# Performance work log

Hardware: AMD Instinct MI355X
Metric: run time of the kernel (lower is better)

The kernel has to match this reference:

```python
import jax, jax.numpy as jnp
import numpy as np
import math

B, L, IN_K, IN_V = 4, 2048, 256, 256
HID, HEADS, OUT = 1024, 8, 256
D = HID // HEADS  # head_dim = 128


def setup_inputs() -> dict:
    key = jax.random.key(0)
    ks = jax.random.split(key, 9)
    s = 0.02
    return {
        "KEY": jax.random.normal(ks[0], (B, L, IN_K), jnp.float32),
        "VALUE": jax.random.normal(ks[1], (B, L, IN_V), jnp.float32),
        "QUERY": jax.random.normal(ks[2], (B, L, IN_K), jnp.float32),
        "W_w": jax.random.normal(ks[3], (HID, IN_K), jnp.float32) * s,
        "W_b": jax.random.normal(ks[4], (HID,), jnp.float32) * s,
        "Wv_w": jax.random.normal(ks[5], (HID, IN_V), jnp.float32) * s,
        "Wv_b": jax.random.normal(ks[6], (HID,), jnp.float32) * s,
        "Wo_w": jax.random.normal(ks[7], (OUT, HID), jnp.float32) * s,
        "Wo_b": jax.random.normal(ks[8], (OUT,), jnp.float32) * s,
    }


def _split_heads(x, b, l):
    # reshape hidden -> (head_dim, num_heads) [head LAST, as in source], then
    # permute(0,3,1,2) -> [B, heads, L, head_dim]
    return x.reshape(b, l, D, HEADS).transpose(0, 3, 1, 2)


def reference(KEY, VALUE, QUERY, W_w, W_b, Wv_w, Wv_b, Wo_w, Wo_b):
    b, lk, _ = KEY.shape
    lq = QUERY.shape[1]
    # shared projection W for KEY and QUERY
    Wk = _split_heads(KEY @ W_w.T + W_b, b, lk)      # [B,h,Lk,d]
    Wq = _split_heads(QUERY @ W_w.T + W_b, b, lq)    # [B,h,Lq,d]
    Wv = _split_heads(VALUE @ Wv_w.T + Wv_b, b, lk)  # [B,h,Lk,d]
    # score[b,h,i,k] = sum_j Wk[b,h,i,j] * Wq[b,h,k,j]
    score = jnp.einsum('bhij,bhkj->bhik', Wk, Wq) / math.sqrt(D)
    # NON-STANDARD: softmax over the HEAD dimension (dim=1)
    attn = jax.nn.softmax(score, axis=1)             # [B,h,Lk,Lq]
    out = jnp.einsum('bhik,bhij->bhjk', attn, Wv)    # [B,h,d,Lq]
    out = out.transpose(0, 2, 1, 3)                  # [B,d,h,Lq]
    out = out.reshape(b, D * HEADS, lq)              # [B,hidden,Lq]
    out = jnp.swapaxes(out, 2, 1)                    # [B,Lq,hidden]
    # dropout is identity in eval mode
    return out @ Wo_w.T + Wo_b                       # [B,Lq,output_size]
```

## Files before the change

### kernel.cpp

```cpp
#include <hip/hip_runtime.h>
#include <hip/hip_bf16.h>
#include <stdint.h>

#define B_    4
#define L_    2048
#define INK   256
#define HID   1024
#define NH    8
#define DH    128
#define OUTF  256

typedef __bf16 v8bf __attribute__((ext_vector_type(8)));
typedef float  v4f  __attribute__((ext_vector_type(4)));

#define MFMA(a,b,c) __builtin_amdgcn_mfma_f32_16x16x32_bf16((a),(b),(c),0,0,0)

__device__ __forceinline__ void gl_lds16(const void* gsrc, void* ldsbase) {
  __builtin_amdgcn_global_load_lds(
      (const __attribute__((address_space(1))) unsigned int*)(uintptr_t)gsrc,
      (__attribute__((address_space(3))) unsigned int*)(uint32_t)(uintptr_t)ldsbase,
      16, 0, 0);
}
__device__ __forceinline__ void barrier_lgkm() {
  asm volatile("s_waitcnt lgkmcnt(0)\n\ts_barrier" ::: "memory");
}

__device__ __forceinline__ unsigned short bfbits(float f) {
  __bf16 h = (__bf16)f;
  return __builtin_bit_cast(unsigned short, h);
}
__device__ __forceinline__ unsigned pack2(float a, float b) {
  return (unsigned)bfbits(a) | ((unsigned)bfbits(b) << 16);
}
__device__ __forceinline__ float bflo(unsigned u) {
  return __builtin_bit_cast(float, u << 16);
}
__device__ __forceinline__ float bfhi(unsigned u) {
  return __builtin_bit_cast(float, u & 0xFFFF0000u);
}

struct ConvArgs {
  const float* src[5];
  __bf16* dst[5];
  int n[5];
};
__global__ __launch_bounds__(256)
void convert_kernel(ConvArgs a) {
  const int r = blockIdx.y;
  const int i = (blockIdx.x * 256 + threadIdx.x) * 4;
  if (i >= a.n[r]) return;
  const float4 v = *(const float4*)(a.src[r] + i);
  uint2 w;
  w.x = pack2(v.x, v.y);
  w.y = pack2(v.z, v.w);
  *reinterpret_cast<uint2*>(a.dst[r] + i) = w;
}

__global__ __launch_bounds__(256)
void wo_perm_kernel(const float* __restrict__ Wo, __bf16* __restrict__ Wop) {
  const int o = blockIdx.x;
  const int hidp = threadIdx.x * 4;
  const int h = hidp >> 7, dd = hidp & 127;
  const float* src = Wo + (size_t)o * HID;
  const float v0 = src[(dd + 0) * 8 + h];
  const float v1 = src[(dd + 1) * 8 + h];
  const float v2 = src[(dd + 2) * 8 + h];
  const float v3 = src[(dd + 3) * 8 + h];
  uint2 w;
  w.x = pack2(v0, v1);
  w.y = pack2(v2, v3);
  *reinterpret_cast<uint2*>(Wop + (size_t)o * HID + hidp) = w;
}

struct ProjArgs {
  const __bf16* X[3];
  const __bf16* W[3];
  const float*  bias[3];
  float scale[3];
  __bf16* out[3];
};
__global__ __launch_bounds__(256, 2)
void proj_kernel(ProjArgs pa)
{
  __shared__ __bf16 sA[2][128 * 64];
  __shared__ __bf16 sB[2][128 * 64];
  const int z = blockIdx.z;
  const __bf16* X = pa.X[z];
  const __bf16* W = pa.W[z];
  const float* bias = pa.bias[z];
  const float scale = pa.scale[z];
  __bf16* out = pa.out[z];
  const int mode = (z == 2);

  const int tid  = threadIdx.x;
  const int lane = tid & 63;
  const int wid  = tid >> 6;
  const int l15  = lane & 15;
  const int q    = lane >> 4;
  const int mblk = blockIdx.x * 128;
  const int nblk = blockIdx.y * 128;

  v4f acc[4][4];
  const v4f vz = {0.f, 0.f, 0.f, 0.f};
#pragma unroll
  for (int i = 0; i < 4; i++)
#pragma unroll
    for (int j = 0; j < 4; j++) acc[i][j] = vz;

  const char* Ab = (const char*)X + (size_t)mblk * 512;
  const char* Bb = (const char*)W + (size_t)nblk * 512;

  auto stage = [&](int p, int c) {
    const int koff = c * 128;
#pragma unroll
    for (int j = 0; j < 4; j++) {
      const int slot = j * 256 + tid;
      const int row = slot >> 3, g = slot & 7;
      gl_lds16(Ab + (size_t)row * 512 + koff + ((g ^ (row & 7)) << 4),
               &sA[p][(j * 256 + wid * 64) * 8]);
    }
#pragma unroll
    for (int j = 0; j < 4; j++) {
      const int slot = j * 256 + tid;
      const int row = slot >> 3, g = slot & 7;
      gl_lds16(Bb + (size_t)row * 512 + koff + ((g ^ (row & 7)) << 4),
               &sB[p][(j * 256 + wid * 64) * 8]);
    }
  };

  stage(0, 0);
  __syncthreads();
#pragma unroll
  for (int c = 0; c < 4; c++) {
    const int p = c & 1;
    if (c + 1 < 4) stage(1 - p, c + 1);
#pragma unroll
    for (int s = 0; s < 2; s++) {
      v8bf a[4], b[4];
#pragma unroll
      for (int t = 0; t < 4; t++) {
        const int row = (wid & 1) * 64 + t * 16 + l15;
        a[t] = *(const v8bf*)&sA[p][(row << 6) + (((s * 4 + q) ^ (row & 7)) << 3)];
      }
#pragma unroll
      for (int t = 0; t < 4; t++) {
        const int row = (wid >> 1) * 64 + t * 16 + l15;
        b[t] = *(const v8bf*)&sB[p][(row << 6) + (((s * 4 + q) ^ (row & 7)) << 3)];
      }
#pragma unroll
      for (int tm = 0; tm < 4; tm++)
#pragma unroll
        for (int tn = 0; tn < 4; tn++)
          acc[tm][tn] = MFMA(a[tm], b[tn], acc[tm][tn]);
    }
    __syncthreads();
  }

#pragma unroll
  for (int tn = 0; tn < 4; tn++) {
    const int n = nblk + (wid >> 1) * 64 + tn * 16 + l15;
    const float bv = bias[n];
    const int h = n & 7;
    const int dd = n >> 3;
#pragma unroll
    for (int tm = 0; tm < 4; tm++)
#pragma unroll
      for (int r = 0; r < 4; r++) {
        const int m = mblk + (wid & 1) * 64 + tm * 16 + q * 4 + r;
        const int b = m >> 11;
        const int i = m & (L_ - 1);
        const float v = (acc[tm][tn][r] + bv) * scale;
        size_t idx;
        if (mode == 0) {
          idx = ((size_t)(b * NH + h) * L_ + i) * DH + dd;
        } else {
          const int ii = (i >> 3) & 3;
          idx = ((size_t)(b * NH + h) * 64 + (i >> 5)) * 4096 +
                (ii * 128 + dd) * 8 + (i & 7);
        }
        out[idx] = (__bf16)v;
      }
  }
}

__global__ __launch_bounds__(512, 2)
void fused_attn_kernel(const __bf16* __restrict__ Kp,
                       const __bf16* __restrict__ Qp,
                       const __bf16* __restrict__ Vg,
                       __bf16* __restrict__ Hd0,
                       __bf16* __restrict__ Hd1)
{
  __shared__ char sPe[32768];

  const int tid  = threadIdx.x;
  const int lane = tid & 63;
  const int h    = tid >> 6;
  const int l15  = lane & 15;
  const int q    = lane >> 4;
  const int k0   = blockIdx.x * 64;
  const int ih   = blockIdx.y;
  const int b    = blockIdx.z;

  const char* KpH = (const char*)Kp + (size_t)(b * NH + h) * L_ * DH * 2;
  const char* QpH = (const char*)Qp + (size_t)(b * NH + h) * L_ * DH * 2;
  const char* VgH = (const char*)Vg + (size_t)(b * NH + h) * 64 * 8192;
  char* sPh = sPe + h * 4096;
  __bf16* Hd = ih ? Hd1 : Hd0;

  v8bf qf[2][2][4];
#pragma unroll
  for (int ks = 0; ks < 2; ks++)
#pragma unroll
    for (int n = 0; n < 2; n++)
#pragma unroll
      for (int c = 0; c < 4; c++)
        qf[ks][n][c] = *(const v8bf*)(QpH +
            (size_t)(k0 + ks * 32 + n * 16 + l15) * 256 + c * 64 + q * 16);

  v4f cacc[8][4];
  const v4f vz = {0.f, 0.f, 0.f, 0.f};
#pragma unroll
  for (int t = 0; t < 8; t++)
#pragma unroll
    for (int n = 0; n < 4; n++) cacc[t][n] = vz;

  const int it0 = ih * 32;
#pragma unroll 1
  for (int itl = 0; itl < 32; ++itl) {
    const int it = it0 + itl;

    v8bf ka[2][4];
    {
      const char* base = KpH + (size_t)it * 32 * 256;
#pragma unroll
      for (int si = 0; si < 2; si++)
#pragma unroll
        for (int c = 0; c < 4; c++)
          ka[si][c] = *(const v8bf*)(base + (si * 16 + l15) * 256 + (c * 4 + q) * 16);
    }

#pragma unroll
    for (int ks = 0; ks < 2; ks++) {
      v4f s[2][2];
#pragma unroll
      for (int si = 0; si < 2; si++)
#pragma unroll
        for (int n = 0; n < 2; n++) s[si][n] = vz;
#pragma unroll
      for (int c = 0; c < 4; c++)
#pragma unroll
        for (int si = 0; si < 2; si++)
#pragma unroll
          for (int n = 0; n < 2; n++)
            s[si][n] = MFMA(ka[si][c], qf[ks][n][c], s[si][n]);
#pragma unroll
      for (int si = 0; si < 2; si++)
#pragma unroll
        for (int n = 0; n < 2; n++) {
          const int kb = ks * 32 + n * 16 + l15;
          const int gi = si * 4 + q;
          uint2 w;
          w.x = pack2(exp2f(s[si][n][0]), exp2f(s[si][n][1]));
          w.y = pack2(exp2f(s[si][n][2]), exp2f(s[si][n][3]));
          *(uint2*)(sPh + kb * 64 + ((gi ^ (kb & 6)) << 3)) = w;
        }
    }
    barrier_lgkm();

    v8bf va[8];
    {
      const char* base = VgH + (size_t)it * 8192 + q * 2048;
#pragma unroll
      for (int t = 0; t < 8; t++)
        va[t] = *(const v8bf*)(base + (t * 16 + l15) * 16);
    }

    {
      const int kk = tid >> 3;
      const int i4 = tid & 7;
      const int off = kk * 64 + ((i4 ^ (kk & 6)) << 3);
      uint2 u[8];
      float s0 = 0.f, s1 = 0.f, s2 = 0.f, s3 = 0.f;
#pragma unroll
      for (int hh = 0; hh < 8; hh++) {
        u[hh] = *(const uint2*)(sPe + hh * 4096 + off);
        s0 += bflo(u[hh].x);
        s1 += bfhi(u[hh].x);
        s2 += bflo(u[hh].y);
        s3 += bfhi(u[hh].y);
      }
      const float r0 = __builtin_amdgcn_rcpf(s0);
      const float r1 = __builtin_amdgcn_rcpf(s1);
      const float r2 = __builtin_amdgcn_rcpf(s2);
      const float r3 = __builtin_amdgcn_rcpf(s3);
#pragma unroll
      for (int hh = 0; hh < 8; hh++) {
        uint2 w;
        w.x = pack2(bflo(u[hh].x) * r0, bfhi(u[hh].x) * r1);
        w.y = pack2(bflo(u[hh].y) * r2, bfhi(u[hh].y) * r3);
        *(uint2*)(sPe + hh * 4096 + off) = w;
      }
    }
    barrier_lgkm();

    v8bf pb[4];
#pragma unroll
    for (int n = 0; n < 4; n++) {
      const int kb = n * 16 + l15;
      pb[n] = *(const v8bf*)(sPh + kb * 64 + (((q * 2) ^ (kb & 6)) << 3));
    }
#pragma unroll
    for (int t = 0; t < 8; t++)
#pragma unroll
      for (int n = 0; n < 4; n++)
        cacc[t][n] = MFMA(va[t], pb[n], cacc[t][n]);
  }

#pragma unroll
  for (int t = 0; t < 8; t++)
#pragma unroll
    for (int n = 0; n < 4; n++) {
      uint2 w;
      w.x = pack2(cacc[t][n][0], cacc[t][n][1]);
      w.y = pack2(cacc[t][n][2], cacc[t][n][3]);
      char* dst = (char*)Hd +
          (((size_t)(b * L_ + k0 + n * 16 + l15)) * HID + h * DH + t * 16 + q * 4) * 2;
      *(uint2*)dst = w;
    }
}

__device__ __forceinline__ v8bf add8(v8bf a, v8bf b) {
  v8bf r;
#pragma unroll
  for (int i = 0; i < 8; i++) r[i] = (__bf16)((float)a[i] + (float)b[i]);
  return r;
}

__global__ __launch_bounds__(256, 2)
void outproj_kernel(const __bf16* __restrict__ Hd0, const __bf16* __restrict__ Hd1,
                    const __bf16* __restrict__ Wop,
                    const float* __restrict__ bo, float* __restrict__ out)
{
  __shared__ __bf16 sA0[2][64 * 64];
  __shared__ __bf16 sA1[2][64 * 64];
  __shared__ __bf16 sB [2][64 * 64];
  const int tid  = threadIdx.x;
  const int lane = tid & 63;
  const int wid  = tid >> 6;
  const int l15  = lane & 15;
  const int q    = lane >> 4;
  const int mblk = blockIdx.x * 64;
  const int nblk = blockIdx.y * 64;

  const char* A0b = (const char*)Hd0 + (size_t)mblk * 2048;
  const char* A1b = (const char*)Hd1 + (size_t)mblk * 2048;
  const char* Bb  = (const char*)Wop + (size_t)nblk * 2048;

  auto stage = [&](int p, int c) {
#pragma unroll
    for (int j = 0; j < 2; j++) {
      const int slot = j * 256 + tid;
      const int row = slot >> 3, g = slot & 7;
      const size_t goff = (size_t)row * 2048 + c * 128 + ((g ^ (row & 7)) << 4);
      gl_lds16(A0b + goff, &sA0[p][(j * 256 + wid * 64) * 8]);
      gl_lds16(A1b + goff, &sA1[p][(j * 256 + wid * 64) * 8]);
      gl_lds16(Bb  + goff, &sB [p][(j * 256 + wid * 64) * 8]);
    }
  };

  v4f acc[2][2];
  const v4f vz = {0.f, 0.f, 0.f, 0.f};
#pragma unroll
  for (int i = 0; i < 2; i++)
#pragma unroll
    for (int j = 0; j < 2; j++) acc[i][j] = vz;

  stage(0, 0);
  __syncthreads();
#pragma unroll 1
  for (int c = 0; c < 16; c++) {
    const int p = c & 1;
    if (c + 1 < 16) stage(1 - p, c + 1);
#pragma unroll
    for (int s = 0; s < 2; s++) {
      v8bf a[2], bb[2];
#pragma unroll
      for (int t = 0; t < 2; t++) {
        const int row = (wid & 1) * 32 + t * 16 + l15;
        const int off = (row << 6) + (((s * 4 + q) ^ (row & 7)) << 3);
        a[t] = add8(*(const v8bf*)&sA0[p][off], *(const v8bf*)&sA1[p][off]);
      }
#pragma unroll
      for (int t = 0; t < 2; t++) {
        const int row = (wid >> 1) * 32 + t * 16 + l15;
        bb[t] = *(const v8bf*)&sB[p][(row << 6) + (((s * 4 + q) ^ (row & 7)) << 3)];
      }
#pragma unroll
      for (int tm = 0; tm < 2; tm++)
#pragma unroll
        for (int tn = 0; tn < 2; tn++)
          acc[tm][tn] = MFMA(a[tm], bb[tn], acc[tm][tn]);
    }
    __syncthreads();
  }

#pragma unroll
  for (int tn = 0; tn < 2; tn++) {
    const int n = nblk + (wid >> 1) * 32 + tn * 16 + l15;
    const float bv = bo[n];
#pragma unroll
    for (int tm = 0; tm < 2; tm++)
#pragma unroll
      for (int r = 0; r < 4; r++) {
        const int m = mblk + (wid & 1) * 32 + tm * 16 + q * 4 + r;
        out[(size_t)m * OUTF + n] = acc[tm][tn][r] + bv;
      }
  }
}

extern "C" void kernel_launch(void* const* d_in, const int* in_sizes, int n_in,
                              void* d_out, int out_size, void* d_ws, size_t ws_size,
                              hipStream_t stream) {
  const float* KEY   = (const float*)d_in[0];
  const float* VALUE = (const float*)d_in[1];
  const float* QUERY = (const float*)d_in[2];
  const float* W_w   = (const float*)d_in[3];
  const float* W_b   = (const float*)d_in[4];
  const float* Wv_w  = (const float*)d_in[5];
  const float* Wv_b  = (const float*)d_in[6];
  const float* Wo_w  = (const float*)d_in[7];
  const float* Wo_b  = (const float*)d_in[8];
  float* out = (float*)d_out;

  const size_t MB = 1024 * 1024;
  char* ws = (char*)d_ws;
  __bf16* Kp  = (__bf16*)(ws);
  __bf16* Qp  = (__bf16*)(ws + 16 * MB);
  __bf16* Vg  = (__bf16*)(ws + 32 * MB);
  __bf16* Hd0 = (__bf16*)(ws + 48 * MB);
  __bf16* Hd1 = (__bf16*)(ws + 64 * MB);
  __bf16* Wop = (__bf16*)(ws + 80 * MB);
  __bf16* Xk  = (__bf16*)(ws + 48 * MB);
  __bf16* Xq  = (__bf16*)(ws + 48 * MB + 4 * MB);
  __bf16* Xv  = (__bf16*)(ws + 48 * MB + 8 * MB);
  __bf16* Wb  = (__bf16*)(ws + 48 * MB + 12 * MB);
  __bf16* Wvb = (__bf16*)(ws + 48 * MB + 12 * MB + 512 * 1024);

  ConvArgs ca;
  ca.src[0] = KEY;   ca.dst[0] = Xk;  ca.n[0] = B_ * L_ * INK;
  ca.src[1] = QUERY; ca.dst[1] = Xq;  ca.n[1] = B_ * L_ * INK;
  ca.src[2] = VALUE; ca.dst[2] = Xv;  ca.n[2] = B_ * L_ * INK;
  ca.src[3] = W_w;   ca.dst[3] = Wb;  ca.n[3] = HID * INK;
  ca.src[4] = Wv_w;  ca.dst[4] = Wvb; ca.n[4] = HID * INK;
  convert_kernel<<<dim3(2048, 5), 256, 0, stream>>>(ca);
  wo_perm_kernel<<<dim3(256), 256, 0, stream>>>(Wo_w, Wop);

  const float c2 = 0.12751744f;
  ProjArgs pa;
  pa.X[0] = Xk;  pa.W[0] = Wb;  pa.bias[0] = W_b;  pa.scale[0] = 1.0f; pa.out[0] = Kp;
  pa.X[1] = Xq;  pa.W[1] = Wb;  pa.bias[1] = W_b;  pa.scale[1] = c2;   pa.out[1] = Qp;
  pa.X[2] = Xv;  pa.W[2] = Wvb; pa.bias[2] = Wv_b; pa.scale[2] = 1.0f; pa.out[2] = Vg;
  proj_kernel<<<dim3(64, 8, 3), 256, 0, stream>>>(pa);

  fused_attn_kernel<<<dim3(32, 2, B_), 512, 0, stream>>>(Kp, Qp, Vg, Hd0, Hd1);

  outproj_kernel<<<dim3(128, 4), 256, 0, stream>>>(Hd0, Hd1, Wop, Wo_b, out);
}
```

Measured before the change: 312.4 us.

## Process two key tiles per barrier round in fused attention kernel

The main loop now handles two 32-key tiles per iteration, storing both sets of exponentiated scores in a doubled LDS buffer of 64 KB of dynamic shared memory. This halves the number of barriers and normalization passes, and the cross-head normalization reads and writes use 16-byte vectors instead of 8-byte ones. In exchange, LDS use per block doubles, which may limit occupancy to one block per CU, and register pressure grows.

```diff
diff --git a/kernel.cpp b/kernel.cpp
--- a/kernel.cpp
+++ b/kernel.cpp
@@ -190,7 +190,7 @@
                        __bf16* __restrict__ Hd0,
                        __bf16* __restrict__ Hd1)
 {
-  __shared__ char sPe[32768];
+  extern __shared__ char sPe[];
 
   const int tid  = threadIdx.x;
   const int lane = tid & 63;
@@ -204,7 +204,7 @@
   const char* KpH = (const char*)Kp + (size_t)(b * NH + h) * L_ * DH * 2;
   const char* QpH = (const char*)Qp + (size_t)(b * NH + h) * L_ * DH * 2;
   const char* VgH = (const char*)Vg + (size_t)(b * NH + h) * 64 * 8192;
-  char* sPh = sPe + h * 4096;
+  char* sPh = sPe + h * 8192;
   __bf16* Hd = ih ? Hd1 : Hd0;
 
   v8bf qf[2][2][4];
@@ -226,94 +226,104 @@
 
   const int it0 = ih * 32;
 #pragma unroll 1
-  for (int itl = 0; itl < 32; ++itl) {
-    const int it = it0 + itl;
-
-    v8bf ka[2][4];
+  for (int r = 0; r < 16; ++r) {
+#pragma unroll
+    for (int sub = 0; sub < 2; ++sub) {
+      const int it = it0 + r * 2 + sub;
+      v8bf ka[2][4];
+      {
+        const char* base = KpH + (size_t)it * 32 * 256;
+#pragma unroll
+        for (int si = 0; si < 2; si++)
+#pragma unroll
+          for (int c = 0; c < 4; c++)
+            ka[si][c] = *(const v8bf*)(base + (si * 16 + l15) * 256 + (c * 4 + q) * 16);
+      }
+#pragma unroll
+      for (int ks = 0; ks < 2; ks++) {
+        v4f s[2][2];
+#pragma unroll
+        for (int si = 0; si < 2; si++)
+#pragma unroll
+          for (int n = 0; n < 2; n++) s[si][n] = vz;
+#pragma unroll
+        for (int c = 0; c < 4; c++)
+#pragma unroll
+          for (int si = 0; si < 2; si++)
+#pragma unroll
+            for (int n = 0; n < 2; n++)
+              s[si][n] = MFMA(ka[si][c], qf[ks][n][c], s[si][n]);
+#pragma unroll
+        for (int si = 0; si < 2; si++)
+#pragma unroll
+          for (int n = 0; n < 2; n++) {
+            const int kb = ks * 32 + n * 16 + l15;
+            const int pg = (sub * 4 + si * 2 + (q >> 1)) ^ (kb & 7);
+            uint2 w;
+            w.x = pack2(exp2f(s[si][n][0]), exp2f(s[si][n][1]));
+            w.y = pack2(exp2f(s[si][n][2]), exp2f(s[si][n][3]));
+            *(uint2*)(sPh + kb * 128 + pg * 16 + (q & 1) * 8) = w;
+          }
+      }
+    }
+    barrier_lgkm();
+
     {
-      const char* base = KpH + (size_t)it * 32 * 256;
-#pragma unroll
-      for (int si = 0; si < 2; si++)
-#pragma unroll
-        for (int c = 0; c < 4; c++)
-          ka[si][c] = *(const v8bf*)(base + (si * 16 + l15) * 256 + (c * 4 + q) * 16);
-    }
-
-#pragma unroll
-    for (int ks = 0; ks < 2; ks++) {
-      v4f s[2][2];
-#pragma unroll
-      for (int si = 0; si < 2; si++)
-#pragma unroll
-        for (int n = 0; n < 2; n++) s[si][n] = vz;
-#pragma unroll
-      for (int c = 0; c < 4; c++)
-#pragma unroll
-        for (int si = 0; si < 2; si++)
-#pragma unroll
-          for (int n = 0; n < 2; n++)
-            s[si][n] = MFMA(ka[si][c], qf[ks][n][c], s[si][n]);
-#pragma unroll
-      for (int si = 0; si < 2; si++)
-#pragma unroll
-        for (int n = 0; n < 2; n++) {
-          const int kb = ks * 32 + n * 16 + l15;
-          const int gi = si * 4 + q;
-          uint2 w;
-          w.x = pack2(exp2f(s[si][n][0]), exp2f(s[si][n][1]));
-          w.y = pack2(exp2f(s[si][n][2]), exp2f(s[si][n][3]));
-          *(uint2*)(sPh + kb * 64 + ((gi ^ (kb & 6)) << 3)) = w;
-        }
-    }
-    barrier_lgkm();
-
-    v8bf va[8];
-    {
-      const char* base = VgH + (size_t)it * 8192 + q * 2048;
-#pragma unroll
-      for (int t = 0; t < 8; t++)
-        va[t] = *(const v8bf*)(base + (t * 16 + l15) * 16);
-    }
-
-    {
-      const int kk = tid >> 3;
-      const int i4 = tid & 7;
-      const int off = kk * 64 + ((i4 ^ (kk & 6)) << 3);
-      uint2 u[8];
+      const int off = (tid >> 3) * 128 + (tid & 7) * 16;
+      uint4 u[8];
       float s0 = 0.f, s1 = 0.f, s2 = 0.f, s3 = 0.f;
+      float s4 = 0.f, s5 = 0.f, s6 = 0.f, s7 = 0.f;
 #pragma unroll
       for (int hh = 0; hh < 8; hh++) {
-        u[hh] = *(const uint2*)(sPe + hh * 4096 + off);
-        s0 += bflo(u[hh].x);
-        s1 += bfhi(u[hh].x);
-        s2 += bflo(u[hh].y);
-        s3 += bfhi(u[hh].y);
+        u[hh] = *(const uint4*)(sPe + hh * 8192 + off);
+        s0 += bflo(u[hh].x); s1 += bfhi(u[hh].x);
+        s2 += bflo(u[hh].y); s3 += bfhi(u[hh].y);
+        s4 += bflo(u[hh].z); s5 += bfhi(u[hh].z);
+        s6 += bflo(u[hh].w); s7 += bfhi(u[hh].w);
       }
       const float r0 = __builtin_amdgcn_rcpf(s0);
       const float r1 = __builtin_amdgcn_rcpf(s1);
       const float r2 = __builtin_amdgcn_rcpf(s2);
       const float r3 = __builtin_amdgcn_rcpf(s3);
+      const float r4 = __builtin_amdgcn_rcpf(s4);
+      const float r5 = __builtin_amdgcn_rcpf(s5);
+      const float r6 = __builtin_amdgcn_rcpf(s6);
+      const float r7 = __builtin_amdgcn_rcpf(s7);
 #pragma unroll
       for (int hh = 0; hh < 8; hh++) {
-        uint2 w;
+        uint4 w;
         w.x = pack2(bflo(u[hh].x) * r0, bfhi(u[hh].x) * r1);
         w.y = pack2(bflo(u[hh].y) * r2, bfhi(u[hh].y) * r3);
-        *(uint2*)(sPe + hh * 4096 + off) = w;
+        w.z = pack2(bflo(u[hh].z) * r4, bfhi(u[hh].z) * r5);
+        w.w = pack2(bflo(u[hh].w) * r6, bfhi(u[hh].w) * r7);
+        *(uint4*)(sPe + hh * 8192 + off) = w;
       }
     }
     barrier_lgkm();
 
-    v8bf pb[4];
-#pragma unroll
-    for (int n = 0; n < 4; n++) {
-      const int kb = n * 16 + l15;
-      pb[n] = *(const v8bf*)(sPh + kb * 64 + (((q * 2) ^ (kb & 6)) << 3));
-    }
-#pragma unroll
-    for (int t = 0; t < 8; t++)
-#pragma unroll
-      for (int n = 0; n < 4; n++)
-        cacc[t][n] = MFMA(va[t], pb[n], cacc[t][n]);
+#pragma unroll
+    for (int sub = 0; sub < 2; ++sub) {
+      const int it = it0 + r * 2 + sub;
+      v8bf va[8];
+      {
+        const char* base = VgH + (size_t)it * 8192 + q * 2048;
+#pragma unroll
+        for (int t = 0; t < 8; t++)
+          va[t] = *(const v8bf*)(base + (t * 16 + l15) * 16);
+      }
+      v8bf pb[4];
+#pragma unroll
+      for (int n = 0; n < 4; n++) {
+        const int kb = n * 16 + l15;
+        const int pg = (sub * 4 + q) ^ (kb & 7);
+        pb[n] = *(const v8bf*)(sPh + kb * 128 + pg * 16);
+      }
+#pragma unroll
+      for (int t = 0; t < 8; t++)
+#pragma unroll
+        for (int n = 0; n < 4; n++)
+          cacc[t][n] = MFMA(va[t], pb[n], cacc[t][n]);
+    }
   }
 
 #pragma unroll
@@ -462,7 +472,7 @@
   pa.X[2] = Xv;  pa.W[2] = Wvb; pa.bias[2] = Wv_b; pa.scale[2] = 1.0f; pa.out[2] = Vg;
   proj_kernel<<<dim3(64, 8, 3), 256, 0, stream>>>(pa);
 
-  fused_attn_kernel<<<dim3(32, 2, B_), 512, 0, stream>>>(Kp, Qp, Vg, Hd0, Hd1);
+  fused_attn_kernel<<<dim3(32, 2, B_), 512, 65536, stream>>>(Kp, Qp, Vg, Hd0, Hd1);
 
   outproj_kernel<<<dim3(128, 4), 256, 0, stream>>>(Hd0, Hd1, Wop, Wo_b, out);
 }
```

Result: slower. 328.8 us (+5.3%).
